# Kernel optimization log

Hardware: AMD Instinct MI355X
Metric: run time of the kernel (lower is better)

## Reference

```python
import jax, jax.numpy as jnp
import numpy as np

N = 50000   # nodes per graph
E = 800000  # edges per graph
FIN = 128   # node_features
H = 4       # heads
C = 32      # out channels per head (hidden_dim // heads)
HID = H * C # 128
FE = 16     # edge_features
B = 8       # graphs in batch
NEG_SLOPE = 0.2


def setup_inputs() -> dict:
    key = jax.random.key(0)
    ks = jax.random.split(key, 30)
    f32 = jnp.float32
    inp = {
        'x_a': jax.random.normal(ks[0], (N, FIN), f32),
        'edge_index_a': jax.random.randint(ks[1], (2, E), 0, N),
        'edge_attr_a': jax.random.normal(ks[2], (E, FE), f32),
        'batch_a': jnp.sort(jax.random.randint(ks[3], (N,), 0, B)),
        'x_b': jax.random.normal(ks[4], (N, FIN), f32),
        'edge_index_b': jax.random.randint(ks[5], (2, E), 0, N),
        'edge_attr_b': jax.random.normal(ks[6], (E, FE), f32),
        'batch_b': jnp.sort(jax.random.randint(ks[7], (N,), 0, B)),
    }
    def p(i, shape, s=0.05):
        return jax.random.normal(ks[i], shape, f32) * s
    # GAT layer 1 (in FIN -> H*C)
    inp['W1l'] = p(8, (FIN, HID)); inp['b1l'] = jnp.zeros((HID,), f32)
    inp['W1r'] = p(9, (FIN, HID)); inp['b1r'] = jnp.zeros((HID,), f32)
    inp['W1e'] = p(10, (FE, HID))
    inp['att1'] = p(11, (H, C))
    inp['bias1'] = jnp.zeros((HID,), f32)
    # GAT layer 2 (in HID -> H*C)
    inp['W2l'] = p(12, (HID, HID)); inp['b2l'] = jnp.zeros((HID,), f32)
    inp['W2r'] = p(13, (HID, HID)); inp['b2r'] = jnp.zeros((HID,), f32)
    inp['W2e'] = p(14, (FE, HID))
    inp['att2'] = p(15, (H, C))
    inp['bias2'] = jnp.zeros((HID,), f32)
    # fc head: Linear(4*HID, HID) -> ReLU -> Linear(HID, 1)
    inp['Wf1'] = p(16, (4 * HID, HID)); inp['bf1'] = jnp.zeros((HID,), f32)
    inp['Wf2'] = p(17, (HID, 1)); inp['bf2'] = jnp.zeros((1,), f32)
    return inp


def gatv2(x, edge_index, edge_attr, Wl, bl, Wr, br, We, att, bias):
    """GATv2Conv (concat=True), eval mode (no dropout)."""
    src, dst = edge_index[0], edge_index[1]
    n = x.shape[0]
    xl = (x @ Wl + bl).reshape(n, H, C)  # source transform
    xr = (x @ Wr + br).reshape(n, H, C)  # target transform
    # per-edge pre-activation: x_j + x_i + edge_emb  -> [E, H, C]
    m = xl[src] + xr[dst] + (edge_attr @ We).reshape(-1, H, C)
    logits = jnp.einsum('ehc,hc->eh', jax.nn.leaky_relu(m, NEG_SLOPE), att)  # [E, H]
    # scatter-softmax over incoming edges of each destination node
    lmax = jax.ops.segment_max(logits, dst, num_segments=n)
    lmax = jnp.where(jnp.isfinite(lmax), lmax, 0.0)
    ex = jnp.exp(logits - lmax[dst])
    denom = jax.ops.segment_sum(ex, dst, num_segments=n)
    alpha = ex / (denom[dst] + 1e-16)  # [E, H]
    out = jax.ops.segment_sum(alpha[:, :, None] * xl[src], dst, num_segments=n)  # [N, H, C]
    return out.reshape(n, HID) + bias


def encode(x, edge_index, edge_attr, batch,
           W1l, b1l, W1r, b1r, W1e, att1, bias1,
           W2l, b2l, W2r, b2r, W2e, att2, bias2):
    h = jax.nn.elu(gatv2(x, edge_index, edge_attr, W1l, b1l, W1r, b1r, W1e, att1, bias1))
    h = jax.nn.elu(gatv2(h, edge_index, edge_attr, W2l, b2l, W2r, b2r, W2e, att2, bias2))
    cnt = jnp.clip(jax.ops.segment_sum(jnp.ones((h.shape[0],), h.dtype), batch, num_segments=B), 1.0)
    h_mean = jax.ops.segment_sum(h, batch, num_segments=B) / cnt[:, None]
    h_max = jax.ops.segment_max(h, batch, num_segments=B)
    h_max = jnp.where(jnp.isfinite(h_max), h_max, 0.0)
    return jnp.concatenate([h_mean, h_max], axis=-1)  # [B, 2*HID]


def reference(x_a, edge_index_a, edge_attr_a, batch_a,
              x_b, edge_index_b, edge_attr_b, batch_b,
              W1l, b1l, W1r, b1r, W1e, att1, bias1,
              W2l, b2l, W2r, b2r, W2e, att2, bias2,
              Wf1, bf1, Wf2, bf2):
    emb_a = encode(x_a, edge_index_a, edge_attr_a, batch_a,
                   W1l, b1l, W1r, b1r, W1e, att1, bias1,
                   W2l, b2l, W2r, b2r, W2e, att2, bias2)
    emb_b = encode(x_b, edge_index_b, edge_attr_b, batch_b,
                   W1l, b1l, W1r, b1r, W1e, att1, bias1,
                   W2l, b2l, W2r, b2r, W2e, att2, bias2)
    combined = jnp.concatenate([emb_a, emb_b], axis=-1)  # [B, 4*HID]
    hidden = jax.nn.relu(combined @ Wf1 + bf1)
    dominance = jax.nn.sigmoid(hidden @ Wf2 + bf2).squeeze(-1)  # [B]
    return dominance
```

## Files before the change

kernel.cpp:

```cpp
#include <hip/hip_runtime.h>
#include <hip/hip_fp16.h>

#define NN 50000
#define NE 800000
#define HIDD 128
#define FEAT_E 16
#define NGRAPH 8
#define CAP 64

typedef __attribute__((ext_vector_type(2))) _Float16 half2_t;
typedef __attribute__((ext_vector_type(8))) _Float16 half8_t;
typedef __attribute__((ext_vector_type(4))) float floatx4;


__device__ __forceinline__ unsigned int fenc(float f) {
  unsigned int u = __float_as_uint(f);
  return (u & 0x80000000u) ? ~u : (u | 0x80000000u);
}
__device__ __forceinline__ float fdec(unsigned int u) {
  if (u == 0u) return 0.0f;
  float f = (u & 0x80000000u) ? __uint_as_float(u & 0x7fffffffu)
                              : __uint_as_float(~u);
  return __builtin_isfinite(f) ? f : 0.0f;
}

__device__ __forceinline__ half8_t splat8(_Float16 v) {
  return (half8_t){v, v, v, v, v, v, v, v};
}
__device__ __forceinline__ half8_t hmax8(half8_t a, half8_t b) {
#if __has_builtin(__builtin_elementwise_max)
  return __builtin_elementwise_max(a, b);
#else
  half8_t r;
#pragma unroll
  for (int i = 0; i < 8; ++i) r[i] = a[i] > b[i] ? a[i] : b[i];
  return r;
#endif
}
__device__ __forceinline__ float dot_att(half8_t lk, half2_t t01, half2_t t23,
                                         half2_t t45, half2_t t67) {
#if __has_builtin(__builtin_amdgcn_fdot2)
  float p = __builtin_amdgcn_fdot2((half2_t){lk[0], lk[1]}, t01, 0.f, false);
  p = __builtin_amdgcn_fdot2((half2_t){lk[2], lk[3]}, t23, p, false);
  p = __builtin_amdgcn_fdot2((half2_t){lk[4], lk[5]}, t45, p, false);
  p = __builtin_amdgcn_fdot2((half2_t){lk[6], lk[7]}, t67, p, false);
  return p;
#else
  float p = 0.f;
  p += (float)lk[0] * (float)t01[0] + (float)lk[1] * (float)t01[1];
  p += (float)lk[2] * (float)t23[0] + (float)lk[3] * (float)t23[1];
  p += (float)lk[4] * (float)t45[0] + (float)lk[5] * (float)t45[1];
  p += (float)lk[6] * (float)t67[0] + (float)lk[7] * (float)t67[1];
  return p;
#endif
}

__global__ void prep_wt_k(const float* __restrict__ Wl, const float* __restrict__ Wr,
                          _Float16* __restrict__ wtg) {
  const int r = blockIdx.x & 127;
  const int which = blockIdx.x >> 7;
  const int k = threadIdx.x;
  const float* W = which ? Wr : Wl;
  const int oc_src = (r & 15) * 8 + (r >> 4);
  const int col = k ^ ((r & 7) << 3);
  wtg[(which * 128 + r) * 128 + col] = (_Float16)W[k * 128 + oc_src];
}

__device__ __forceinline__ half8_t load_a8(const _Float16* p) {
  return *(const half8_t*)p;
}
__device__ __forceinline__ half8_t load_a8(const float* p) {
  const float4 f0 = *(const float4*)p;
  const float4 f1 = *(const float4*)(p + 4);
  return (half8_t){(_Float16)f0.x, (_Float16)f0.y, (_Float16)f0.z, (_Float16)f0.w,
                   (_Float16)f1.x, (_Float16)f1.y, (_Float16)f1.z, (_Float16)f1.w};
}

template <typename TIN>
__global__ __launch_bounds__(256) void node_linear_mfma_k(
    const TIN* __restrict__ x, const _Float16* __restrict__ wtg,
    const float* __restrict__ bl, const float* __restrict__ br,
    _Float16* __restrict__ xl16, _Float16* __restrict__ xr16) {
  __shared__ _Float16 wt[128 * 128];
  const int tid = threadIdx.x;
  const int which = blockIdx.y;
  const _Float16* wsrc = wtg + which * (128 * 128);
  const float* bias128 = which ? br : bl;
  _Float16* out = which ? xr16 : xl16;
  {
    const half8_t* src = (const half8_t*)wsrc;
    half8_t* dstl = (half8_t*)wt;
#pragma unroll
    for (int it = 0; it < 8; ++it)
      dstl[it * 256 + tid] = src[it * 256 + tid];
  }
  __syncthreads();

  const int wv = tid >> 6, lane = tid & 63;
  const int arow = lane & 15, kq = lane >> 4;
  const int nbase = blockIdx.x * 64 + wv * 16;
  int nload = nbase + arow;
  if (nload >= NN) nload = NN - 1;
  floatx4 acc[8];
#pragma unroll
  for (int t = 0; t < 8; ++t) acc[t] = (floatx4){0.f, 0.f, 0.f, 0.f};
#pragma unroll
  for (int kb = 0; kb < 4; ++kb) {
    const half8_t a = load_a8(x + (size_t)nload * 128 + kb * 32 + kq * 8);
    const int colbase = (kb * 32 + kq * 8) ^ ((arow & 7) << 3);
#pragma unroll
    for (int t = 0; t < 8; ++t) {
      const half8_t b = *(const half8_t*)&wt[(t * 16 + arow) * 128 + colbase];
      acc[t] = __builtin_amdgcn_mfma_f32_16x16x32_f16(a, b, acc[t], 0, 0, 0);
    }
  }
  const float4 bv0 = *(const float4*)&bias128[arow * 8];
  const float4 bv1 = *(const float4*)&bias128[arow * 8 + 4];
  const float bv[8] = {bv0.x, bv0.y, bv0.z, bv0.w, bv1.x, bv1.y, bv1.z, bv1.w};
#pragma unroll
  for (int i = 0; i < 4; ++i) {
    const int n = nbase + kq * 4 + i;
    if (n < NN) {
      half8_t v;
#pragma unroll
      for (int t = 0; t < 8; ++t) v[t] = (_Float16)(acc[t][i] + bv[t]);
      *(half8_t*)(out + (size_t)n * 128 + arow * 8) = v;
    }
  }
}

__global__ void build_k(const int* __restrict__ src, const int* __restrict__ dst,
                        const float* __restrict__ eattr,
                        int* __restrict__ cnt, int2* __restrict__ bpair,
                        _Float16* __restrict__ eatt16) {
  const int e = blockIdx.x * blockDim.x + threadIdx.x;
  if (e >= NE) return;
  const float4* ea = (const float4*)(eattr + (size_t)e * FEAT_E);
  const float4 a0 = ea[0], a1 = ea[1], a2 = ea[2], a3 = ea[3];
  half8_t h0 = {(_Float16)a0.x, (_Float16)a0.y, (_Float16)a0.z, (_Float16)a0.w,
                (_Float16)a1.x, (_Float16)a1.y, (_Float16)a1.z, (_Float16)a1.w};
  half8_t h1 = {(_Float16)a2.x, (_Float16)a2.y, (_Float16)a2.z, (_Float16)a2.w,
                (_Float16)a3.x, (_Float16)a3.y, (_Float16)a3.z, (_Float16)a3.w};
  half8_t* eo = (half8_t*)(eatt16 + (size_t)e * FEAT_E);
  eo[0] = h0; eo[1] = h1;
  const int d = dst[e];
  const int pos = atomicAdd(&cnt[d], 1);
  if (pos < CAP) bpair[(size_t)d * CAP + pos] = make_int2(src[e], e);
}

__global__ __launch_bounds__(256) void node_gat_fused_k(
    const _Float16* __restrict__ xl16, const _Float16* __restrict__ xr16,
    const _Float16* __restrict__ eatt16,
    const int2* __restrict__ bpair, const int* __restrict__ cnt,
    const float* __restrict__ We, const float* __restrict__ att,
    const float* __restrict__ bias, _Float16* __restrict__ hout) {
  __shared__ half8_t WeS[FEAT_E][16];
  const int tid = threadIdx.x;
  {
    const int f = tid >> 4, q = tid & 15;
    const float4 w0 = ((const float4*)We)[f * 32 + q * 2];
    const float4 w1 = ((const float4*)We)[f * 32 + q * 2 + 1];
    WeS[f][q] = (half8_t){(_Float16)w0.x, (_Float16)w0.y, (_Float16)w0.z, (_Float16)w0.w,
                          (_Float16)w1.x, (_Float16)w1.y, (_Float16)w1.z, (_Float16)w1.w};
  }
  __syncthreads();

  const int wave = tid >> 6, lane = tid & 63;
  const int slot = lane >> 4, l16 = lane & 15;
  const int d = blockIdx.x * 4 + wave;

  const float4 af0 = ((const float4*)att)[l16 * 2];
  const float4 af1 = ((const float4*)att)[l16 * 2 + 1];
  const half2_t at01 = {(_Float16)af0.x, (_Float16)af0.y};
  const half2_t at23 = {(_Float16)af0.z, (_Float16)af0.w};
  const half2_t at45 = {(_Float16)af1.x, (_Float16)af1.y};
  const half2_t at67 = {(_Float16)af1.z, (_Float16)af1.w};

  const half8_t xrh = *(const half8_t*)(xr16 + (size_t)d * HIDD + l16 * 8);

  int deg = cnt[d];
  deg = deg < CAP ? deg : CAP;

  int2 myp = make_int2(0, 0);
  if (lane < deg) myp = bpair[(size_t)d * CAP + lane];

  float acc0 = 0.f, acc1 = 0.f, acc2 = 0.f, acc3 = 0.f;
  float acc4 = 0.f, acc5 = 0.f, acc6 = 0.f, acc7 = 0.f;
  float den = 0.f;

#define FINISH_EDGE(XL, EM, VALID)                                       \
  {                                                                      \
    half8_t m_ = ((XL) + xrh) + (EM);                                    \
    half8_t lk_ = hmax8(m_, m_ * splat8((_Float16)0.2f));                \
    float p_ = dot_att(lk_, at01, at23, at45, at67);                     \
    p_ += __shfl_xor(p_, 1);                                             \
    p_ += __shfl_xor(p_, 2);                                             \
    const float w_ = (VALID) ? __expf(p_) : 0.f;                         \
    den += w_;                                                           \
    acc0 = fmaf(w_, (float)(XL)[0], acc0);                               \
    acc1 = fmaf(w_, (float)(XL)[1], acc1);                               \
    acc2 = fmaf(w_, (float)(XL)[2], acc2);                               \
    acc3 = fmaf(w_, (float)(XL)[3], acc3);                               \
    acc4 = fmaf(w_, (float)(XL)[4], acc4);                               \
    acc5 = fmaf(w_, (float)(XL)[5], acc5);                               \
    acc6 = fmaf(w_, (float)(XL)[6], acc6);                               \
    acc7 = fmaf(w_, (float)(XL)[7], acc7);                               \
  }

#define LOAD_PAIR_AT(E0, E1, X0, X1, A0, B0, A1, B1)                     \
  {                                                                      \
    const int s0_ = __shfl(myp.x, (E0)), i0_ = __shfl(myp.y, (E0));      \
    const int s1_ = __shfl(myp.x, (E1)), i1_ = __shfl(myp.y, (E1));      \
    X0 = *(const half8_t*)(xl16 + (unsigned)s0_ * 128u + l16 * 8);       \
    X1 = *(const half8_t*)(xl16 + (unsigned)s1_ * 128u + l16 * 8);       \
    A0 = *(const half8_t*)(eatt16 + (unsigned)i0_ * 16u);                \
    B0 = *(const half8_t*)(eatt16 + (unsigned)i0_ * 16u + 8u);           \
    A1 = *(const half8_t*)(eatt16 + (unsigned)i1_ * 16u);                \
    B1 = *(const half8_t*)(eatt16 + (unsigned)i1_ * 16u + 8u);           \
  }

#define COMPUTE_PAIR()                                                   \
  {                                                                      \
    half8_t em0 = {}, em1 = {};                                          \
    _Pragma("unroll") for (int f = 0; f < 8; ++f) {                      \
      const half8_t wf = WeS[f][l16];                                    \
      em0 += splat8(a0[f]) * wf;                                         \
      em1 += splat8(a1[f]) * wf;                                         \
    }                                                                    \
    _Pragma("unroll") for (int f = 0; f < 8; ++f) {                      \
      const half8_t wf = WeS[8 + f][l16];                                \
      em0 += splat8(b0[f]) * wf;                                         \
      em1 += splat8(b1[f]) * wf;                                         \
    }                                                                    \
    FINISH_EDGE(x0, em0, e0 < deg)                                       \
    FINISH_EDGE(x1, em1, e1 < deg)                                       \
  }

  const int T = (deg + 7) >> 3;
  if (T > 0) {
    int e0 = slot, e1 = slot + 4;
    half8_t x0, x1, a0, b0, a1, b1;
    LOAD_PAIR_AT(e0, e1, x0, x1, a0, b0, a1, b1)
    for (int k = 0; k + 1 < T; ++k) {
      half8_t nx0, nx1, na0, nb0, na1, nb1;
      LOAD_PAIR_AT(e0 + 8, e1 + 8, nx0, nx1, na0, nb0, na1, nb1)
      COMPUTE_PAIR()
      e0 += 8; e1 += 8;
      x0 = nx0; x1 = nx1; a0 = na0; b0 = nb0; a1 = na1; b1 = nb1;
    }
    const bool pairLast = (((T - 1) << 3) + 4) < deg;
    if (pairLast) {
      COMPUTE_PAIR()
    } else {
      half8_t em0 = {};
#pragma unroll
      for (int f = 0; f < 8; ++f) em0 += splat8(a0[f]) * WeS[f][l16];
#pragma unroll
      for (int f = 0; f < 8; ++f) em0 += splat8(b0[f]) * WeS[8 + f][l16];
      FINISH_EDGE(x0, em0, e0 < deg)
    }
  }
#undef COMPUTE_PAIR
#undef LOAD_PAIR_AT
#undef FINISH_EDGE

#define RED(A) A += __shfl_xor(A, 16); A += __shfl_xor(A, 32);
  RED(acc0) RED(acc1) RED(acc2) RED(acc3)
  RED(acc4) RED(acc5) RED(acc6) RED(acc7)
  RED(den)
#undef RED
  if (slot == 0) {
    const float inv = 1.f / (den + 1e-16f);
    const float4 b0 = ((const float4*)bias)[l16 * 2];
    const float4 b1 = ((const float4*)bias)[l16 * 2 + 1];
    float o0 = fmaf(acc0, inv, b0.x), o1 = fmaf(acc1, inv, b0.y);
    float o2 = fmaf(acc2, inv, b0.z), o3 = fmaf(acc3, inv, b0.w);
    float o4 = fmaf(acc4, inv, b1.x), o5 = fmaf(acc5, inv, b1.y);
    float o6 = fmaf(acc6, inv, b1.z), o7 = fmaf(acc7, inv, b1.w);
    o0 = o0 > 0.f ? o0 : expm1f(o0);  o1 = o1 > 0.f ? o1 : expm1f(o1);
    o2 = o2 > 0.f ? o2 : expm1f(o2);  o3 = o3 > 0.f ? o3 : expm1f(o3);
    o4 = o4 > 0.f ? o4 : expm1f(o4);  o5 = o5 > 0.f ? o5 : expm1f(o5);
    o6 = o6 > 0.f ? o6 : expm1f(o6);  o7 = o7 > 0.f ? o7 : expm1f(o7);
    half8_t ho = {(_Float16)o0, (_Float16)o1, (_Float16)o2, (_Float16)o3,
                  (_Float16)o4, (_Float16)o5, (_Float16)o6, (_Float16)o7};
    *(half8_t*)(hout + (size_t)d * HIDD + l16 * 8) = ho;
  }
}

__global__ void pool_k(const _Float16* __restrict__ h, const int* __restrict__ batch,
                       float* __restrict__ gsum, unsigned int* __restrict__ gmax,
                       float* __restrict__ gcnt) {
  __shared__ float ssum[NGRAPH][HIDD];
  __shared__ float smax[NGRAPH][HIDD];
  __shared__ float scnt[NGRAPH];
  const int t = threadIdx.x;
#pragma unroll
  for (int g = 0; g < NGRAPH; ++g) {
    ssum[g][t] = 0.f;
    smax[g][t] = -3.0e38f;
  }
  if (t < NGRAPH) scnt[t] = 0.f;
  __syncthreads();
  const int n0 = blockIdx.x * 64;
  const int nEnd = (n0 + 64 < NN) ? (n0 + 64) : NN;
  unsigned int seen = 0;
  for (int n = n0; n < nEnd; ++n) {
    const int g = batch[n];
    seen |= 1u << g;
    const float v = (float)h[(size_t)n * HIDD + t];
    ssum[g][t] += v;
    smax[g][t] = fmaxf(smax[g][t], v);
    if (t == 0) scnt[g] += 1.f;
  }
  __syncthreads();
  for (int g = 0; g < NGRAPH; ++g) {
    if (seen & (1u << g)) {
      atomicAdd(&gsum[g * HIDD + t], ssum[g][t]);
      atomicMax(&gmax[g * HIDD + t], fenc(smax[g][t]));
      if (t == 0) atomicAdd(&gcnt[g], scnt[g]);
    }
  }
}

__global__ void head_k(const float* __restrict__ suma, const unsigned int* __restrict__ maxa,
                       const float* __restrict__ cnta,
                       const float* __restrict__ sumb, const unsigned int* __restrict__ maxb,
                       const float* __restrict__ cntb,
                       const float* __restrict__ Wf1, const float* __restrict__ bf1,
                       const float* __restrict__ Wf2, const float* __restrict__ bf2,
                       float* __restrict__ out) {
  __shared__ float c[4 * HIDD];
  __shared__ float red[HIDD];
  const int g = blockIdx.x, t = threadIdx.x;
  const float ca = fmaxf(cnta[g], 1.f), cb = fmaxf(cntb[g], 1.f);
  c[t]            = suma[g * HIDD + t] / ca;
  c[HIDD + t]     = fdec(maxa[g * HIDD + t]);
  c[2 * HIDD + t] = sumb[g * HIDD + t] / cb;
  c[3 * HIDD + t] = fdec(maxb[g * HIDD + t]);
  __syncthreads();
  float acc = bf1[t];
  for (int i = 0; i < 4 * HIDD; ++i)
    acc = fmaf(c[i], Wf1[(size_t)i * HIDD + t], acc);
  acc = fmaxf(acc, 0.f);
  red[t] = acc * Wf2[t];
  __syncthreads();
  for (int s2 = 64; s2 > 0; s2 >>= 1) {
    if (t < s2) red[t] += red[t + s2];
    __syncthreads();
  }
  if (t == 0) out[g] = 1.f / (1.f + expf(-(red[0] + bf2[0])));
}

extern "C" void kernel_launch(void* const* d_in, const int* in_sizes, int n_in,
                              void* d_out, int out_size, void* d_ws, size_t ws_size,
                              hipStream_t stream) {
  (void)in_sizes; (void)n_in; (void)out_size; (void)ws_size;
  const float* xA    = (const float*)d_in[0];
  const int*   eiA   = (const int*)  d_in[1];
  const float* eaA   = (const float*)d_in[2];
  const int*   batA  = (const int*)  d_in[3];
  const float* xB    = (const float*)d_in[4];
  const int*   eiB   = (const int*)  d_in[5];
  const float* eaB   = (const float*)d_in[6];
  const int*   batB  = (const int*)  d_in[7];
  const float* W1l   = (const float*)d_in[8];
  const float* b1l   = (const float*)d_in[9];
  const float* W1r   = (const float*)d_in[10];
  const float* b1r   = (const float*)d_in[11];
  const float* W1e   = (const float*)d_in[12];
  const float* att1  = (const float*)d_in[13];
  const float* bias1 = (const float*)d_in[14];
  const float* W2l   = (const float*)d_in[15];
  const float* b2l   = (const float*)d_in[16];
  const float* W2r   = (const float*)d_in[17];
  const float* b2r   = (const float*)d_in[18];
  const float* W2e   = (const float*)d_in[19];
  const float* att2  = (const float*)d_in[20];
  const float* bias2 = (const float*)d_in[21];
  const float* Wf1   = (const float*)d_in[22];
  const float* bf1   = (const float*)d_in[23];
  const float* Wf2   = (const float*)d_in[24];
  const float* bf2   = (const float*)d_in[25];

  char* ws = (char*)d_ws;
  size_t off = 0;
  auto alloc = [&](size_t bytes) -> void* {
    void* p = ws + off;
    off += (bytes + 255) & ~(size_t)255;
    return p;
  };
  _Float16* h16    = (_Float16*)alloc((size_t)NN * HIDD * 2);
  _Float16* xl16   = (_Float16*)alloc((size_t)NN * HIDD * 2);
  _Float16* xr16   = (_Float16*)alloc((size_t)NN * HIDD * 2);
  int2*     bpair  = (int2*)    alloc((size_t)NN * CAP * 8);
  _Float16* eatt16 = (_Float16*)alloc((size_t)NE * FEAT_E * 2);
  int*      cnt    = (int*)     alloc((size_t)NN * 4);
  _Float16* wtg1   = (_Float16*)alloc(2 * 128 * 128 * 2);
  _Float16* wtg2   = (_Float16*)alloc(2 * 128 * 128 * 2);
  const size_t poolStart = off;
  float*        psumA = (float*)alloc(NGRAPH * HIDD * 4);
  unsigned int* pmaxA = (unsigned int*)alloc(NGRAPH * HIDD * 4);
  float*        pcntA = (float*)alloc(NGRAPH * 4);
  float*        psumB = (float*)alloc(NGRAPH * HIDD * 4);
  unsigned int* pmaxB = (unsigned int*)alloc(NGRAPH * HIDD * 4);
  float*        pcntB = (float*)alloc(NGRAPH * 4);
  const size_t poolBytes = off - poolStart;

  const float* xs[2]   = {xA, xB};
  const int*   eis[2]  = {eiA, eiB};
  const float* eas[2]  = {eaA, eaB};
  const int*   bats[2] = {batA, batB};
  float*        psums[2] = {psumA, psumB};
  unsigned int* pmaxs[2] = {pmaxA, pmaxB};
  float*        pcnts[2] = {pcntA, pcntB};

  hipMemsetAsync(psumA, 0, poolBytes, stream);
  prep_wt_k<<<256, 128, 0, stream>>>(W1l, W1r, wtg1);
  prep_wt_k<<<256, 128, 0, stream>>>(W2l, W2r, wtg2);

  for (int g = 0; g < 2; ++g) {
    const int* src = eis[g];
    const int* dst = eis[g] + NE;
    hipMemsetAsync(cnt, 0, (size_t)NN * 4, stream);
    build_k<<<NE / 256, 256, 0, stream>>>(src, dst, eas[g], cnt, bpair, eatt16);
    node_linear_mfma_k<float><<<dim3((NN + 63) / 64, 2), 256, 0, stream>>>(
        xs[g], wtg1, b1l, b1r, xl16, xr16);
    node_gat_fused_k<<<NN / 4, 256, 0, stream>>>(xl16, xr16, eatt16, bpair, cnt,
                                                 W1e, att1, bias1, h16);
    node_linear_mfma_k<_Float16><<<dim3((NN + 63) / 64, 2), 256, 0, stream>>>(
        h16, wtg2, b2l, b2r, xl16, xr16);
    node_gat_fused_k<<<NN / 4, 256, 0, stream>>>(xl16, xr16, eatt16, bpair, cnt,
                                                 W2e, att2, bias2, h16);
    pool_k<<<(NN + 63) / 64, 128, 0, stream>>>(h16, bats[g], psums[g], pmaxs[g], pcnts[g]);
  }
  head_k<<<NGRAPH, 128, 0, stream>>>(psumA, pmaxA, pcntA, psumB, pmaxB, pcntB,
                                     Wf1, bf1, Wf2, bf2, (float*)d_out);
}
```

Baseline: 797.4 us.

## Make GAT aggregation kernel persistent with prefetch of next node's metadata

The per-node GAT aggregation kernel becomes a grid-stride persistent kernel with a fixed 1280 blocks. Each wave loops over nodes strided by the total wave count. While it processes the current node's edges, it prefetches the next node's degree, edge-pair list and xr row. Bias loads and the We staging into shared memory are now done once per block instead of once per node. The aim is to hide the dependent cnt→bpair→gather latency chain and cut per-block launch and setup overhead, at the cost of higher register pressure and possibly worse load balance across waves.

```diff
diff --git a/kernel.cpp b/kernel.cpp
--- a/kernel.cpp
+++ b/kernel.cpp
@@ -7,6 +7,7 @@
 #define FEAT_E 16
 #define NGRAPH 8
 #define CAP 64
+#define GATBLK 1280
 
 typedef __attribute__((ext_vector_type(2))) _Float16 half2_t;
 typedef __attribute__((ext_vector_type(8))) _Float16 half8_t;
@@ -167,7 +168,7 @@
 
   const int wave = tid >> 6, lane = tid & 63;
   const int slot = lane >> 4, l16 = lane & 15;
-  const int d = blockIdx.x * 4 + wave;
+  constexpr int NW = GATBLK * 4;
 
   const float4 af0 = ((const float4*)att)[l16 * 2];
   const float4 af1 = ((const float4*)att)[l16 * 2 + 1];
@@ -175,18 +176,18 @@
   const half2_t at23 = {(_Float16)af0.z, (_Float16)af0.w};
   const half2_t at45 = {(_Float16)af1.x, (_Float16)af1.y};
   const half2_t at67 = {(_Float16)af1.z, (_Float16)af1.w};
-
-  const half8_t xrh = *(const half8_t*)(xr16 + (size_t)d * HIDD + l16 * 8);
-
-  int deg = cnt[d];
-  deg = deg < CAP ? deg : CAP;
-
-  int2 myp = make_int2(0, 0);
-  if (lane < deg) myp = bpair[(size_t)d * CAP + lane];
-
-  float acc0 = 0.f, acc1 = 0.f, acc2 = 0.f, acc3 = 0.f;
-  float acc4 = 0.f, acc5 = 0.f, acc6 = 0.f, acc7 = 0.f;
-  float den = 0.f;
+  const float4 bi0 = ((const float4*)bias)[l16 * 2];
+  const float4 bi1 = ((const float4*)bias)[l16 * 2 + 1];
+
+  int d = blockIdx.x * 4 + wave;
+  int degA = cnt[d];
+  degA = degA < CAP ? degA : CAP;
+  int dB = d + NW;
+  int degB_raw = 0;
+  if (dB < NN) degB_raw = cnt[dB];
+  int2 mypA = make_int2(0, 0);
+  if (lane < degA) mypA = bpair[(size_t)d * CAP + lane];
+  half8_t xrhA = *(const half8_t*)(xr16 + (size_t)d * HIDD + l16 * 8);
 
 #define FINISH_EDGE(XL, EM, VALID)                                       \
   {                                                                      \
@@ -236,55 +237,78 @@
     FINISH_EDGE(x1, em1, e1 < deg)                                       \
   }
 
-  const int T = (deg + 7) >> 3;
-  if (T > 0) {
+  for (;;) {
+    const int deg = degA;
+    const int2 myp = mypA;
+    const half8_t xrh = xrhA;
+    float acc0 = 0.f, acc1 = 0.f, acc2 = 0.f, acc3 = 0.f;
+    float acc4 = 0.f, acc5 = 0.f, acc6 = 0.f, acc7 = 0.f;
+    float den = 0.f;
+
+    const int T = (deg + 7) >> 3;
     int e0 = slot, e1 = slot + 4;
     half8_t x0, x1, a0, b0, a1, b1;
-    LOAD_PAIR_AT(e0, e1, x0, x1, a0, b0, a1, b1)
-    for (int k = 0; k + 1 < T; ++k) {
-      half8_t nx0, nx1, na0, nb0, na1, nb1;
-      LOAD_PAIR_AT(e0 + 8, e1 + 8, nx0, nx1, na0, nb0, na1, nb1)
-      COMPUTE_PAIR()
-      e0 += 8; e1 += 8;
-      x0 = nx0; x1 = nx1; a0 = na0; b0 = nb0; a1 = na1; b1 = nb1;
-    }
-    const bool pairLast = (((T - 1) << 3) + 4) < deg;
-    if (pairLast) {
-      COMPUTE_PAIR()
-    } else {
-      half8_t em0 = {};
-#pragma unroll
-      for (int f = 0; f < 8; ++f) em0 += splat8(a0[f]) * WeS[f][l16];
-#pragma unroll
-      for (int f = 0; f < 8; ++f) em0 += splat8(b0[f]) * WeS[8 + f][l16];
-      FINISH_EDGE(x0, em0, e0 < deg)
-    }
+    if (T > 0) {
+      LOAD_PAIR_AT(e0, e1, x0, x1, a0, b0, a1, b1)
+    }
+    const int dC = dB + NW;
+    int degB = degB_raw < CAP ? degB_raw : CAP;
+    int degC_raw = 0;
+    int2 mypB = make_int2(0, 0);
+    half8_t xrhB = {};
+    if (dB < NN) {
+      if (dC < NN) degC_raw = cnt[dC];
+      if (lane < degB) mypB = bpair[(size_t)dB * CAP + lane];
+      xrhB = *(const half8_t*)(xr16 + (size_t)dB * HIDD + l16 * 8);
+    }
+    if (T > 0) {
+      for (int k = 0; k + 1 < T; ++k) {
+        half8_t nx0, nx1, na0, nb0, na1, nb1;
+        LOAD_PAIR_AT(e0 + 8, e1 + 8, nx0, nx1, na0, nb0, na1, nb1)
+        COMPUTE_PAIR()
+        e0 += 8; e1 += 8;
+        x0 = nx0; x1 = nx1; a0 = na0; b0 = nb0; a1 = na1; b1 = nb1;
+      }
+      const bool pairLast = (((T - 1) << 3) + 4) < deg;
+      if (pairLast) {
+        COMPUTE_PAIR()
+      } else {
+        half8_t em0 = {};
+#pragma unroll
+        for (int f = 0; f < 8; ++f) em0 += splat8(a0[f]) * WeS[f][l16];
+#pragma unroll
+        for (int f = 0; f < 8; ++f) em0 += splat8(b0[f]) * WeS[8 + f][l16];
+        FINISH_EDGE(x0, em0, e0 < deg)
+      }
+    }
+
+#define RED(A) A += __shfl_xor(A, 16); A += __shfl_xor(A, 32);
+    RED(acc0) RED(acc1) RED(acc2) RED(acc3)
+    RED(acc4) RED(acc5) RED(acc6) RED(acc7)
+    RED(den)
+#undef RED
+    if (slot == 0) {
+      const float inv = 1.f / (den + 1e-16f);
+      float o0 = fmaf(acc0, inv, bi0.x), o1 = fmaf(acc1, inv, bi0.y);
+      float o2 = fmaf(acc2, inv, bi0.z), o3 = fmaf(acc3, inv, bi0.w);
+      float o4 = fmaf(acc4, inv, bi1.x), o5 = fmaf(acc5, inv, bi1.y);
+      float o6 = fmaf(acc6, inv, bi1.z), o7 = fmaf(acc7, inv, bi1.w);
+      o0 = o0 > 0.f ? o0 : expm1f(o0);  o1 = o1 > 0.f ? o1 : expm1f(o1);
+      o2 = o2 > 0.f ? o2 : expm1f(o2);  o3 = o3 > 0.f ? o3 : expm1f(o3);
+      o4 = o4 > 0.f ? o4 : expm1f(o4);  o5 = o5 > 0.f ? o5 : expm1f(o5);
+      o6 = o6 > 0.f ? o6 : expm1f(o6);  o7 = o7 > 0.f ? o7 : expm1f(o7);
+      half8_t ho = {(_Float16)o0, (_Float16)o1, (_Float16)o2, (_Float16)o3,
+                    (_Float16)o4, (_Float16)o5, (_Float16)o6, (_Float16)o7};
+      *(half8_t*)(hout + (size_t)d * HIDD + l16 * 8) = ho;
+    }
+
+    if (dB >= NN) break;
+    d = dB; degA = degB; mypA = mypB; xrhA = xrhB;
+    dB = dC; degB_raw = degC_raw;
   }
 #undef COMPUTE_PAIR
 #undef LOAD_PAIR_AT
 #undef FINISH_EDGE
-
-#define RED(A) A += __shfl_xor(A, 16); A += __shfl_xor(A, 32);
-  RED(acc0) RED(acc1) RED(acc2) RED(acc3)
-  RED(acc4) RED(acc5) RED(acc6) RED(acc7)
-  RED(den)
-#undef RED
-  if (slot == 0) {
-    const float inv = 1.f / (den + 1e-16f);
-    const float4 b0 = ((const float4*)bias)[l16 * 2];
-    const float4 b1 = ((const float4*)bias)[l16 * 2 + 1];
-    float o0 = fmaf(acc0, inv, b0.x), o1 = fmaf(acc1, inv, b0.y);
-    float o2 = fmaf(acc2, inv, b0.z), o3 = fmaf(acc3, inv, b0.w);
-    float o4 = fmaf(acc4, inv, b1.x), o5 = fmaf(acc5, inv, b1.y);
-    float o6 = fmaf(acc6, inv, b1.z), o7 = fmaf(acc7, inv, b1.w);
-    o0 = o0 > 0.f ? o0 : expm1f(o0);  o1 = o1 > 0.f ? o1 : expm1f(o1);
-    o2 = o2 > 0.f ? o2 : expm1f(o2);  o3 = o3 > 0.f ? o3 : expm1f(o3);
-    o4 = o4 > 0.f ? o4 : expm1f(o4);  o5 = o5 > 0.f ? o5 : expm1f(o5);
-    o6 = o6 > 0.f ? o6 : expm1f(o6);  o7 = o7 > 0.f ? o7 : expm1f(o7);
-    half8_t ho = {(_Float16)o0, (_Float16)o1, (_Float16)o2, (_Float16)o3,
-                  (_Float16)o4, (_Float16)o5, (_Float16)o6, (_Float16)o7};
-    *(half8_t*)(hout + (size_t)d * HIDD + l16 * 8) = ho;
-  }
 }
 
 __global__ void pool_k(const _Float16* __restrict__ h, const int* __restrict__ batch,
@@ -425,11 +449,11 @@
     build_k<<<NE / 256, 256, 0, stream>>>(src, dst, eas[g], cnt, bpair, eatt16);
     node_linear_mfma_k<float><<<dim3((NN + 63) / 64, 2), 256, 0, stream>>>(
         xs[g], wtg1, b1l, b1r, xl16, xr16);
-    node_gat_fused_k<<<NN / 4, 256, 0, stream>>>(xl16, xr16, eatt16, bpair, cnt,
+    node_gat_fused_k<<<GATBLK, 256, 0, stream>>>(xl16, xr16, eatt16, bpair, cnt,
                                                  W1e, att1, bias1, h16);
     node_linear_mfma_k<_Float16><<<dim3((NN + 63) / 64, 2), 256, 0, stream>>>(
         h16, wtg2, b2l, b2r, xl16, xr16);
-    node_gat_fused_k<<<NN / 4, 256, 0, stream>>>(xl16, xr16, eatt16, bpair, cnt,
+    node_gat_fused_k<<<GATBLK, 256, 0, stream>>>(xl16, xr16, eatt16, bpair, cnt,
                                                  W2e, att2, bias2, h16);
     pool_k<<<(NN + 63) / 64, 128, 0, stream>>>(h16, bats[g], psums[g], pmaxs[g], pcnts[g]);
   }
```

Measured after the change: 800.0 us. Within noise of the previous version (+0.3%).
